# Optimization experiments

Hardware: AMD Instinct MI355X
Metric: run time of the kernel (lower is better)

## Reference

```python
import jax, jax.numpy as jnp
import numpy as np

B, S, K, N = 4, 2048, 4096, 4096   # batch, seq, infeatures, outfeatures
GROUP = 128                        # quantization group size along K
N_OUT = 128                        # outlier features (last columns of x)


def setup_inputs() -> dict:
    key = jax.random.key(0)
    ks = jax.random.split(key, 6)
    x = jax.random.normal(ks[0], (B, S, K), dtype=jnp.float32)
    # unpacked 4-bit integer weights in [0, 16)
    qweight = jax.random.randint(ks[1], (N, K), 0, 16, dtype=jnp.int32)
    # per-group scales and scaled zeros: [numgroup, N] = [K//GROUP, N]
    scales = jax.random.uniform(ks[2], (K // GROUP, N), dtype=jnp.float32, minval=0.005, maxval=0.02)
    # scaled_zeros = -zeros * scales in the original pack(); keep them negative-ish
    scaled_zeros = -jax.random.uniform(ks[3], (K // GROUP, N), dtype=jnp.float32, minval=0.0, maxval=0.16)
    oweight = jax.random.normal(ks[4], (N, N_OUT), dtype=jnp.float32) * 0.02
    bias = jax.random.normal(ks[5], (N,), dtype=jnp.float32) * 0.02
    return {"x": x, "qweight": qweight, "scales": scales,
            "scaled_zeros": scaled_zeros, "oweight": oweight, "bias": bias}


def reference(x, qweight, scales, scaled_zeros, oweight, bias):
    # gemm_4bit: dequantize W[n,k] = q[n,k]*scales[k//G, n] + scaled_zeros[k//G, n]
    g = x.shape[-1] // scales.shape[0]
    scales_full = jnp.repeat(scales, g, axis=0).T        # [N, K]
    zeros_full = jnp.repeat(scaled_zeros, g, axis=0).T   # [N, K]
    W = qweight.astype(scales.dtype) * scales_full + zeros_full  # [N, K]
    y = jnp.einsum('bsk,nk->bsn', x, W)
    # fused outlier fp16 linear on the last N_OUT input features + bias
    n_out = oweight.shape[1]
    y = y + jnp.einsum('bso,no->bsn', x[..., -n_out:], oweight) + bias
    return y
```

## Files before the change

kernel.cpp:

```cpp
#include <hip/hip_runtime.h>

#define K_ 4096
#define N_ 4096
#define M_ 8192
#define NOUT_ 128

typedef __bf16 bf16x8 __attribute__((ext_vector_type(8)));
typedef float f32x4 __attribute__((ext_vector_type(4)));
typedef unsigned short ushort8 __attribute__((ext_vector_type(8)));

__device__ __forceinline__ unsigned short f2bf(float f) {
  unsigned u = __builtin_bit_cast(unsigned, f);
  u += 0x7fffu + ((u >> 16) & 1u);
  return (unsigned short)(u >> 16);
}

__global__ void cvt_x_kernel(const float4* __restrict__ x4, ushort8* __restrict__ xb) {
  const int t = blockIdx.x * 256 + threadIdx.x;
  float4 a = x4[2 * t];
  float4 b = x4[2 * t + 1];
  ushort8 o;
  o[0] = f2bf(a.x); o[1] = f2bf(a.y); o[2] = f2bf(a.z); o[3] = f2bf(a.w);
  o[4] = f2bf(b.x); o[5] = f2bf(b.y); o[6] = f2bf(b.z); o[7] = f2bf(b.w);
  xb[t] = o;
}

__global__ void dequant_kernel(const int4* __restrict__ q4,
                               const float* __restrict__ scales,
                               const float* __restrict__ zeros,
                               const float* __restrict__ ow,
                               ushort8* __restrict__ wb) {
  const int t = blockIdx.x * 256 + threadIdx.x;
  const int n = t >> 9;
  const int k = (t & 511) << 3;
  const int g = k >> 7;
  const float s = scales[g * N_ + n];
  const float z = zeros[g * N_ + n];
  int4 qa = q4[2 * t], qb = q4[2 * t + 1];
  float f[8];
  f[0] = qa.x * s + z; f[1] = qa.y * s + z; f[2] = qa.z * s + z; f[3] = qa.w * s + z;
  f[4] = qb.x * s + z; f[5] = qb.y * s + z; f[6] = qb.z * s + z; f[7] = qb.w * s + z;
  if (k >= K_ - NOUT_) {
    const float4* o4 = (const float4*)(ow + n * NOUT_ + (k - (K_ - NOUT_)));
    float4 oa = o4[0], ob = o4[1];
    f[0] += oa.x; f[1] += oa.y; f[2] += oa.z; f[3] += oa.w;
    f[4] += ob.x; f[5] += ob.y; f[6] += ob.z; f[7] += ob.w;
  }
  ushort8 r;
  #pragma unroll
  for (int i = 0; i < 8; ++i) r[i] = f2bf(f[i]);
  wb[t] = r;
}

__global__ __launch_bounds__(256, 3) void gemm_kernel(
    const unsigned short* __restrict__ xb,
    const unsigned short* __restrict__ wb,
    const float* __restrict__ bias,
    float* __restrict__ out) {
  __shared__ char sA[16384];
  __shared__ char sB[16384];

  const int tid  = threadIdx.x;
  const int w    = tid >> 6;
  const int lane = tid & 63;
  const int q    = lane >> 4;
  const int l16  = lane & 15;
  const int x7   = l16 & 7;
  const int wr   = w >> 1;
  const int wc   = w & 1;

  const int m0 = blockIdx.y * 128;
  const int n0 = blockIdx.x * 128;

  const unsigned short* gA[4];
  const unsigned short* gB[4];
  char* ldsA[4];
  char* ldsB[4];
  #pragma unroll
  for (int i = 0; i < 4; ++i) {
    const int o  = i * 4096 + w * 1024 + lane * 16;
    const int r  = o >> 7;
    const int cs = (o >> 4) & 7;
    const int cg = cs ^ (r & 7);
    gA[i] = xb + (size_t)(m0 + r) * K_ + cg * 8;
    gB[i] = wb + (size_t)(n0 + r) * K_ + cg * 8;
    ldsA[i] = sA + i * 4096 + w * 1024;
    ldsB[i] = sB + i * 4096 + w * 1024;
  }

  const char* pA = sA + (wr * 64 + l16) * 128;
  const char* pB = sB + (wc * 64 + l16) * 128;
  const int slot0 = ((0 + q) ^ x7) * 16;
  const int slot1 = ((4 + q) ^ x7) * 16;

  f32x4 acc[4][4] = {};

  for (int kt = 0; kt < K_ / 64; ++kt) {
    const int kof = kt * 64;
    #pragma unroll
    for (int i = 0; i < 4; ++i)
      __builtin_amdgcn_global_load_lds(
          (__attribute__((address_space(1))) void*)(gA[i] + kof),
          (__attribute__((address_space(3))) void*)ldsA[i], 16, 0, 0);
    #pragma unroll
    for (int i = 0; i < 4; ++i)
      __builtin_amdgcn_global_load_lds(
          (__attribute__((address_space(1))) void*)(gB[i] + kof),
          (__attribute__((address_space(3))) void*)ldsB[i], 16, 0, 0);
    __syncthreads();

    #pragma unroll
    for (int s = 0; s < 2; ++s) {
      const int slot = s ? slot1 : slot0;
      bf16x8 a[4], b[4];
      #pragma unroll
      for (int i = 0; i < 4; ++i)
        a[i] = *(const bf16x8*)(pA + i * 2048 + slot);
      #pragma unroll
      for (int j = 0; j < 4; ++j)
        b[j] = *(const bf16x8*)(pB + j * 2048 + slot);
      #pragma unroll
      for (int i = 0; i < 4; ++i)
        #pragma unroll
        for (int j = 0; j < 4; ++j)
          acc[i][j] = __builtin_amdgcn_mfma_f32_16x16x32_bf16(a[i], b[j], acc[i][j], 0, 0, 0);
    }
    __syncthreads();
  }

  float bv[4];
  #pragma unroll
  for (int j = 0; j < 4; ++j)
    bv[j] = bias[n0 + wc * 64 + j * 16 + l16];

  #pragma unroll
  for (int i = 0; i < 4; ++i) {
    const int mrow = m0 + wr * 64 + i * 16 + q * 4;
    #pragma unroll
    for (int j = 0; j < 4; ++j) {
      const int n = n0 + wc * 64 + j * 16 + l16;
      float* op = out + (size_t)mrow * N_ + n;
      #pragma unroll
      for (int r = 0; r < 4; ++r)
        op[(size_t)r * N_] = acc[i][j][r] + bv[j];
    }
  }
}

extern "C" void kernel_launch(void* const* d_in, const int* in_sizes, int n_in,
                              void* d_out, int out_size, void* d_ws, size_t ws_size,
                              hipStream_t stream) {
  const float* x      = (const float*)d_in[0];
  const int*   qw     = (const int*)d_in[1];
  const float* scales = (const float*)d_in[2];
  const float* zeros  = (const float*)d_in[3];
  const float* ow     = (const float*)d_in[4];
  const float* bias   = (const float*)d_in[5];
  float* out = (float*)d_out;

  unsigned short* xb = (unsigned short*)d_ws;
  unsigned short* wb = xb + (size_t)M_ * K_;

  cvt_x_kernel<<<(M_ * K_ / 8) / 256, 256, 0, stream>>>((const float4*)x, (ushort8*)xb);
  dequant_kernel<<<(N_ * K_ / 8) / 256, 256, 0, stream>>>((const int4*)qw, scales, zeros, ow,
                                                          (ushort8*)wb);
  dim3 grid(N_ / 128, M_ / 128);
  gemm_kernel<<<grid, 256, 0, stream>>>(xb, wb, bias, out);
}
```

Baseline: 531.1 us.

## Switch GEMM to 32x32x16 bf16 MFMA with fragment-ordered LDS layout

Replaces the 16x16x32 MFMA tiling (4x4 accumulators per wave) with 32x32x16 MFMA (2x2 f32x16 accumulators). The LDS staging layout is reorganized so each lane's operand fragment for a k-step sits contiguously at lane*16, which removes the XOR swizzle. The goal is fewer MFMA issues and fewer LDS reads per flop. The risk is LDS bank conflicts, because the unswizzled global_load_lds layout changes the access pattern, and the larger MFMA has different latency and scheduling behaviour.

```diff
diff --git a/kernel.cpp b/kernel.cpp
--- a/kernel.cpp
+++ b/kernel.cpp
@@ -6,7 +6,7 @@
 #define NOUT_ 128
 
 typedef __bf16 bf16x8 __attribute__((ext_vector_type(8)));
-typedef float f32x4 __attribute__((ext_vector_type(4)));
+typedef float f32x16 __attribute__((ext_vector_type(16)));
 typedef unsigned short ushort8 __attribute__((ext_vector_type(8)));
 
 __device__ __forceinline__ unsigned short f2bf(float f) {
@@ -63,9 +63,6 @@
   const int tid  = threadIdx.x;
   const int w    = tid >> 6;
   const int lane = tid & 63;
-  const int q    = lane >> 4;
-  const int l16  = lane & 15;
-  const int x7   = l16 & 7;
   const int wr   = w >> 1;
   const int wc   = w & 1;
 
@@ -77,72 +74,69 @@
   char* ldsA[4];
   char* ldsB[4];
   #pragma unroll
-  for (int i = 0; i < 4; ++i) {
-    const int o  = i * 4096 + w * 1024 + lane * 16;
-    const int r  = o >> 7;
-    const int cs = (o >> 4) & 7;
-    const int cg = cs ^ (r & 7);
-    gA[i] = xb + (size_t)(m0 + r) * K_ + cg * 8;
-    gB[i] = wb + (size_t)(n0 + r) * K_ + cg * 8;
-    ldsA[i] = sA + i * 4096 + w * 1024;
-    ldsB[i] = sB + i * 4096 + w * 1024;
+  for (int p = 0; p < 4; ++p) {
+    const int o = w * 4096 + p * 1024 + lane * 16;
+    const int s = o >> 12;
+    const int i = (o >> 10) & 3;
+    const int h = (o >> 9) & 1;
+    const int r = (o >> 4) & 31;
+    const int kc = (s * 2 + h) * 8;
+    gA[p] = xb + (size_t)(m0 + i * 32 + r) * K_ + kc;
+    gB[p] = wb + (size_t)(n0 + i * 32 + r) * K_ + kc;
+    ldsA[p] = sA + w * 4096 + p * 1024;
+    ldsB[p] = sB + w * 4096 + p * 1024;
   }
 
-  const char* pA = sA + (wr * 64 + l16) * 128;
-  const char* pB = sB + (wc * 64 + l16) * 128;
-  const int slot0 = ((0 + q) ^ x7) * 16;
-  const int slot1 = ((4 + q) ^ x7) * 16;
+  const char* pA = sA + wr * 2048 + lane * 16;
+  const char* pB = sB + wc * 2048 + lane * 16;
 
-  f32x4 acc[4][4] = {};
+  f32x16 acc[2][2] = {};
 
   for (int kt = 0; kt < K_ / 64; ++kt) {
     const int kof = kt * 64;
     #pragma unroll
-    for (int i = 0; i < 4; ++i)
+    for (int p = 0; p < 4; ++p)
       __builtin_amdgcn_global_load_lds(
-          (__attribute__((address_space(1))) void*)(gA[i] + kof),
-          (__attribute__((address_space(3))) void*)ldsA[i], 16, 0, 0);
+          (__attribute__((address_space(1))) void*)(gA[p] + kof),
+          (__attribute__((address_space(3))) void*)ldsA[p], 16, 0, 0);
     #pragma unroll
-    for (int i = 0; i < 4; ++i)
+    for (int p = 0; p < 4; ++p)
       __builtin_amdgcn_global_load_lds(
-          (__attribute__((address_space(1))) void*)(gB[i] + kof),
-          (__attribute__((address_space(3))) void*)ldsB[i], 16, 0, 0);
+          (__attribute__((address_space(1))) void*)(gB[p] + kof),
+          (__attribute__((address_space(3))) void*)ldsB[p], 16, 0, 0);
     __syncthreads();
 
     #pragma unroll
-    for (int s = 0; s < 2; ++s) {
-      const int slot = s ? slot1 : slot0;
-      bf16x8 a[4], b[4];
-      #pragma unroll
-      for (int i = 0; i < 4; ++i)
-        a[i] = *(const bf16x8*)(pA + i * 2048 + slot);
-      #pragma unroll
-      for (int j = 0; j < 4; ++j)
-        b[j] = *(const bf16x8*)(pB + j * 2048 + slot);
-      #pragma unroll
-      for (int i = 0; i < 4; ++i)
-        #pragma unroll
-        for (int j = 0; j < 4; ++j)
-          acc[i][j] = __builtin_amdgcn_mfma_f32_16x16x32_bf16(a[i], b[j], acc[i][j], 0, 0, 0);
+    for (int s = 0; s < 4; ++s) {
+      bf16x8 a0 = *(const bf16x8*)(pA + s * 4096);
+      bf16x8 a1 = *(const bf16x8*)(pA + s * 4096 + 1024);
+      bf16x8 b0 = *(const bf16x8*)(pB + s * 4096);
+      bf16x8 b1 = *(const bf16x8*)(pB + s * 4096 + 1024);
+      acc[0][0] = __builtin_amdgcn_mfma_f32_32x32x16_bf16(a0, b0, acc[0][0], 0, 0, 0);
+      acc[0][1] = __builtin_amdgcn_mfma_f32_32x32x16_bf16(a0, b1, acc[0][1], 0, 0, 0);
+      acc[1][0] = __builtin_amdgcn_mfma_f32_32x32x16_bf16(a1, b0, acc[1][0], 0, 0, 0);
+      acc[1][1] = __builtin_amdgcn_mfma_f32_32x32x16_bf16(a1, b1, acc[1][1], 0, 0, 0);
     }
     __syncthreads();
   }
 
-  float bv[4];
-  #pragma unroll
-  for (int j = 0; j < 4; ++j)
-    bv[j] = bias[n0 + wc * 64 + j * 16 + l16];
+  const int l31 = lane & 31;
+  const int lh  = lane >> 5;
+  float bv[2];
+  bv[0] = bias[n0 + wc * 64 + l31];
+  bv[1] = bias[n0 + wc * 64 + 32 + l31];
 
   #pragma unroll
-  for (int i = 0; i < 4; ++i) {
-    const int mrow = m0 + wr * 64 + i * 16 + q * 4;
+  for (int i2 = 0; i2 < 2; ++i2) {
+    const int mb = m0 + wr * 64 + i2 * 32 + 4 * lh;
     #pragma unroll
-    for (int j = 0; j < 4; ++j) {
-      const int n = n0 + wc * 64 + j * 16 + l16;
-      float* op = out + (size_t)mrow * N_ + n;
+    for (int j2 = 0; j2 < 2; ++j2) {
+      const int n = n0 + wc * 64 + j2 * 32 + l31;
       #pragma unroll
-      for (int r = 0; r < 4; ++r)
-        op[(size_t)r * N_] = acc[i][j][r] + bv[j];
+      for (int reg = 0; reg < 16; ++reg) {
+        const int row = mb + (reg & 3) + 8 * (reg >> 2);
+        out[(size_t)row * N_ + n] = acc[i2][j2][reg] + bv[j2];
+      }
     }
   }
 }
```

After: 739.1 us. +39.1%, slower.
